# Kernel optimization log

Hardware: AMD Instinct MI355X
Metric: run time of the kernel (lower is better)

## Reference

```python
import jax, jax.numpy as jnp
import numpy as np

N = 50000      # nodes
E = 800000     # edges (before self loops)
H = 4          # heads
C_IN = 128     # input feature dim
C_HID = 64     # per-head out channels (hidden_dim == output_dim)
SLOPE = 0.2    # GATConv leaky_relu negative slope


def setup_inputs() -> dict:
    key = jax.random.key(0)
    ks = jax.random.split(key, 16)
    x = jax.random.normal(ks[0], (N, C_IN), jnp.float32)
    edge_index = jax.random.randint(ks[1], (2, E), 0, N, jnp.int32)

    def p(k, shape):
        return jax.random.normal(k, shape, jnp.float32) * 0.05

    inp = {"x": x, "edge_index": edge_index}
    in_dims = [C_IN, C_HID, C_HID]
    for i in range(3):
        inp[f"W{i+1}"] = p(ks[2 + 4 * i], (in_dims[i], H * C_HID))
        inp[f"asrc{i+1}"] = p(ks[3 + 4 * i], (H, C_HID))
        inp[f"adst{i+1}"] = p(ks[4 + 4 * i], (H, C_HID))
        inp[f"b{i+1}"] = jnp.zeros((C_HID,), jnp.float32)
    return inp


def _gat_layer(x, src, dst, W, a_s, a_d, b):
    # x: [N, F_in]; src/dst: [E'] (self loops included)
    n = x.shape[0]
    h = (x @ W).reshape(n, H, -1)                      # [N, H, C]
    alpha_src = jnp.einsum('nhc,hc->nh', h, a_s)       # att_src . h  (source side)
    alpha_dst = jnp.einsum('nhc,hc->nh', h, a_d)       # att_dst . h  (target side)
    e = jax.nn.leaky_relu(alpha_src[src] + alpha_dst[dst], SLOPE)  # [E', H]
    # scatter-softmax over incoming edges of each dst node
    m = jax.ops.segment_max(e, dst, num_segments=n)    # [N, H]
    ex = jnp.exp(e - m[dst])
    denom = jax.ops.segment_sum(ex, dst, num_segments=n)
    alpha = ex / (denom[dst] + 1e-16)                  # [E', H]
    # scatter-add aggregation of weighted source features
    out = jax.ops.segment_sum(alpha[:, :, None] * h[src], dst, num_segments=n)  # [N, H, C]
    return out.mean(axis=1) + b                        # concat=False -> head mean, + bias


def reference(x, edge_index, W1, asrc1, adst1, b1, W2, asrc2, adst2, b2,
              W3, asrc3, adst3, b3):
    n = x.shape[0]
    loops = jnp.arange(n, dtype=edge_index.dtype)      # GATConv add_self_loops=True
    src = jnp.concatenate([edge_index[0], loops])
    dst = jnp.concatenate([edge_index[1], loops])
    for W, a_s, a_d, b in ((W1, asrc1, adst1, b1),
                           (W2, asrc2, adst2, b2),
                           (W3, asrc3, adst3, b3)):
        x = jax.nn.relu(_gat_layer(x, src, dst, W, a_s, a_d, b))
    return x
```

## Files before the change

kernel.cpp:

```cpp
#include <hip/hip_runtime.h>
#include <hip/hip_bf16.h>
#include <cstddef>

#define NH 4
#define CHID 64
#define HC 256

typedef __attribute__((ext_vector_type(8))) short bf16x8;
typedef __attribute__((ext_vector_type(4))) float f32x4;


__global__ void hist_kernel(const int* __restrict__ ei, int E, int N,
                            int* __restrict__ deg) {
  int i = blockIdx.x * blockDim.x + threadIdx.x;
  int EP = E + N;
  if (i >= EP) return;
  int d = (i < E) ? ei[E + i] : (i - E);
  atomicAdd(&deg[d], 1);
}

__global__ __launch_bounds__(256) void partial_sum_kernel(const int* __restrict__ deg,
                                                          int* __restrict__ part, int n) {
  __shared__ int red[4];
  int t = threadIdx.x;
  int i = blockIdx.x * 256 + t;
  int v = (i < n) ? deg[i] : 0;
#pragma unroll
  for (int o = 32; o; o >>= 1) v += __shfl_xor(v, o, 64);
  if ((t & 63) == 0) red[t >> 6] = v;
  __syncthreads();
  if (t == 0) part[blockIdx.x] = red[0] + red[1] + red[2] + red[3];
}

__global__ __launch_bounds__(256) void scan_part_kernel(int* __restrict__ part, int nb,
                                                        int* __restrict__ row_off, int n) {
  __shared__ int s[256];
  int t = threadIdx.x;
  int v = (t < nb) ? part[t] : 0;
  s[t] = v;
  __syncthreads();
  for (int o = 1; o < 256; o <<= 1) {
    int u = (t >= o) ? s[t - o] : 0;
    __syncthreads();
    s[t] += u;
    __syncthreads();
  }
  if (t < nb) part[t] = s[t] - v;
  if (t == 255) row_off[n] = s[255];
}

__global__ __launch_bounds__(256) void row_off_kernel(const int* __restrict__ deg,
                                                      const int* __restrict__ part,
                                                      int* __restrict__ row_off, int n) {
  __shared__ int s[256];
  int t = threadIdx.x;
  int i = blockIdx.x * 256 + t;
  int v = (i < n) ? deg[i] : 0;
  s[t] = v;
  __syncthreads();
  for (int o = 1; o < 256; o <<= 1) {
    int u = (t >= o) ? s[t - o] : 0;
    __syncthreads();
    s[t] += u;
    __syncthreads();
  }
  if (i < n) row_off[i] = part[blockIdx.x] + s[t] - v;
}

__global__ void scatter_kernel(const int* __restrict__ ei, int E, int N,
                               const int* __restrict__ row_off,
                               int* __restrict__ cursor, int* __restrict__ ssrc,
                               int* __restrict__ sdst) {
  int i = blockIdx.x * blockDim.x + threadIdx.x;
  int EP = E + N;
  if (i >= EP) {
    if (i < EP + 8) { ssrc[i] = 0; sdst[i] = 0; }
    return;
  }
  int s, d;
  if (i < E) { s = ei[i]; d = ei[E + i]; } else { s = i - E; d = s; }
  int pos = row_off[d] + atomicAdd(&cursor[d], 1);
  ssrc[pos] = s;
  sdst[pos] = d;
}


__global__ void prep_kernel(const float* __restrict__ x,
                            __hip_bfloat16* __restrict__ xhi,
                            __hip_bfloat16* __restrict__ xlo, int n4,
                            const float* __restrict__ W1, const float* __restrict__ W2,
                            const float* __restrict__ W3,
                            __hip_bfloat16* __restrict__ w1hi,
                            __hip_bfloat16* __restrict__ w2hi,
                            __hip_bfloat16* __restrict__ w3hi) {
  int i = blockIdx.x * blockDim.x + threadIdx.x;
  if (i < n4) {
    float4 v = reinterpret_cast<const float4*>(x)[i];
    __hip_bfloat16 h[4], l[4];
    float f[4] = {v.x, v.y, v.z, v.w};
#pragma unroll
    for (int j = 0; j < 4; ++j) {
      h[j] = __float2bfloat16(f[j]);
      l[j] = __float2bfloat16(f[j] - __bfloat162float(h[j]));
    }
    reinterpret_cast<uint2*>(xhi)[i] = *reinterpret_cast<uint2*>(h);
    reinterpret_cast<uint2*>(xlo)[i] = *reinterpret_cast<uint2*>(l);
    return;
  }
  int j = i - n4;
  if (j >= 65536) return;
  const float* W; __hip_bfloat16* hi; int K, base;
  if (j < 32768)      { W = W1; hi = w1hi; K = 128; base = j; }
  else if (j < 49152) { W = W2; hi = w2hi; K = 64;  base = j - 32768; }
  else                { W = W3; hi = w3hi; K = 64;  base = j - 49152; }
  int k = base >> 8;
  int c = base & 255;
  hi[c * K + k] = __float2bfloat16(W[base]);
}


template <int K>
__global__ __launch_bounds__(256) void gemm_mfma_kernel(
    const __hip_bfloat16* __restrict__ Ahi, const __hip_bfloat16* __restrict__ Alo,
    const __hip_bfloat16* __restrict__ Bthi,
    const float* __restrict__ a_s, const float* __restrict__ a_d,
    __hip_bfloat16* __restrict__ h, float* __restrict__ asrc_n,
    float* __restrict__ adst_n, int n_rows, int row_groups) {
  extern __shared__ char smem[];
  uint4* lds4 = reinterpret_cast<uint4*>(smem);
  constexpr int KS = K / 32;
  constexpr int S16 = (128 * K * 2) >> 4;
  constexpr int rowshift = (K == 128) ? 4 : 3;
  int ch = blockIdx.y;
  int colbase = ch * 128;

  {
    const uint4* g = reinterpret_cast<const uint4*>(Bthi + (size_t)colbase * K);
    for (int c = threadIdx.x; c < S16; c += 256) {
      int row = c >> rowshift;
      lds4[c ^ (row & 7)] = g[c];
    }
  }
  __syncthreads();

  int wave = threadIdx.x >> 6;
  int lane = threadIdx.x & 63;
  int n16  = lane & 15;
  int g4   = lane >> 4;
  const bf16x8 z8 = {0, 0, 0, 0, 0, 0, 0, 0};

  for (int gg = blockIdx.x; gg < row_groups; gg += gridDim.x) {
    int row0 = gg * 64 + wave * 16;
    int xrow = row0 + n16;
    bool aval = xrow < n_rows;
    size_t xbase = (size_t)xrow * K + g4 * 8;

    bf16x8 xh[KS], xl[KS];
#pragma unroll
    for (int s = 0; s < KS; ++s) {
      xh[s] = aval ? *reinterpret_cast<const bf16x8*>(&Ahi[xbase + s * 32]) : z8;
      xl[s] = aval ? *reinterpret_cast<const bf16x8*>(&Alo[xbase + s * 32]) : z8;
    }

    f32x4 acc[8];
#pragma unroll
    for (int ct = 0; ct < 8; ++ct) acc[ct] = (f32x4){0.f, 0.f, 0.f, 0.f};

#pragma unroll
    for (int ct = 0; ct < 8; ++ct) {
      int wrow = ct * 16 + n16;
#pragma unroll
      for (int s = 0; s < KS; ++s) {
        int ci = ((wrow * K + s * 32 + g4 * 8) >> 3) ^ (wrow & 7);
        bf16x8 wh = *reinterpret_cast<const bf16x8*>(&lds4[ci]);
        acc[ct] = __builtin_amdgcn_mfma_f32_16x16x32_bf16(wh, xh[s], acc[ct], 0, 0, 0);
        acc[ct] = __builtin_amdgcn_mfma_f32_16x16x32_bf16(wh, xl[s], acc[ct], 0, 0, 0);
      }
    }

    int r = row0 + n16;
    bool valid = r < n_rows;

    if (valid) {
#pragma unroll
      for (int ct = 0; ct < 8; ++ct) {
        unsigned short u[4];
#pragma unroll
        for (int i = 0; i < 4; ++i) {
          __hip_bfloat16 b = __float2bfloat16(acc[ct][i]);
          u[i] = *reinterpret_cast<unsigned short*>(&b);
        }
        *reinterpret_cast<uint2*>(&h[(size_t)r * HC + colbase + ct * 16 + g4 * 4]) =
            *reinterpret_cast<uint2*>(u);
      }
    }

    float ps[2] = {0.f, 0.f};
    float pd[2] = {0.f, 0.f};
#pragma unroll
    for (int ct = 0; ct < 8; ++ct) {
      int hh = ct >> 2;
      int col = colbase + ct * 16 + g4 * 4;
      float4 as4 = *reinterpret_cast<const float4*>(&a_s[col]);
      float4 ad4 = *reinterpret_cast<const float4*>(&a_d[col]);
      ps[hh] += acc[ct][0] * as4.x + acc[ct][1] * as4.y + acc[ct][2] * as4.z + acc[ct][3] * as4.w;
      pd[hh] += acc[ct][0] * ad4.x + acc[ct][1] * ad4.y + acc[ct][2] * ad4.z + acc[ct][3] * ad4.w;
    }
#pragma unroll
    for (int hh = 0; hh < 2; ++hh) {
      ps[hh] += __shfl_xor(ps[hh], 16, 64);
      ps[hh] += __shfl_xor(ps[hh], 32, 64);
      pd[hh] += __shfl_xor(pd[hh], 16, 64);
      pd[hh] += __shfl_xor(pd[hh], 32, 64);
    }
    if (lane < 16 && valid) {
      *reinterpret_cast<float2*>(&asrc_n[(size_t)r * NH + ch * 2]) =
          make_float2(ps[0], ps[1]);
      *reinterpret_cast<float2*>(&adst_n[(size_t)r * NH + ch * 2]) =
          make_float2(pd[0], pd[1]);
    }
  }
}


__global__ void edge_weight_kernel(const int* __restrict__ ssrc, const int* __restrict__ sdst,
                                   const float* __restrict__ asrc_n,
                                   const float* __restrict__ adst_n,
                                   float4* __restrict__ wbuf, int EP) {
  int i = blockIdx.x * blockDim.x + threadIdx.x;
  if (i >= EP) {
    if (i < EP + 8) wbuf[i] = make_float4(0.f, 0.f, 0.f, 0.f);
    return;
  }
  int s = ssrc[i];
  int d = sdst[i];
  float4 a = reinterpret_cast<const float4*>(asrc_n)[s];
  float4 b = reinterpret_cast<const float4*>(adst_n)[d];
  float e0 = a.x + b.x; e0 = (e0 > 0.f) ? e0 : 0.2f * e0;
  float e1 = a.y + b.y; e1 = (e1 > 0.f) ? e1 : 0.2f * e1;
  float e2 = a.z + b.z; e2 = (e2 > 0.f) ? e2 : 0.2f * e2;
  float e3 = a.w + b.w; e3 = (e3 > 0.f) ? e3 : 0.2f * e3;
  wbuf[i] = make_float4(__expf(e0), __expf(e1), __expf(e2), __expf(e3));
}


__global__ __launch_bounds__(256) void aggregate_kernel(
    const int* __restrict__ row_off, const int* __restrict__ ssrc,
    const __hip_bfloat16* __restrict__ h, const float4* __restrict__ wbuf,
    const float* __restrict__ bias,
    __hip_bfloat16* __restrict__ out_hi, __hip_bfloat16* __restrict__ out_lo,
    float* __restrict__ out_f32, int n_nodes) {
  int n = (blockIdx.x * blockDim.x + threadIdx.x) >> 6;
  if (n >= n_nodes) return;
  int l    = threadIdx.x & 63;
  int slot = l >> 3;
  int cp   = l & 7;
  const char* hbase = reinterpret_cast<const char*>(h);
  const float4 z4 = make_float4(0.f, 0.f, 0.f, 0.f);
  const uint4 zu = {0, 0, 0, 0};

  int beg  = row_off[n];
  int deg  = row_off[n + 1] - beg;

  float facc[32];
#pragma unroll
  for (int u = 0; u < 32; ++u) facc[u] = 0.f;
  float4 ds = z4;

  auto LOADE = [&](int j, float4& w4, uint4* d) {
    int jj  = j + slot;
    int idx = beg + jj;
    int sv  = ssrc[idx];
    float4 w = wbuf[idx];
    bool ok = jj < deg;
    w4.x = ok ? w.x : 0.f;
    w4.y = ok ? w.y : 0.f;
    w4.z = ok ? w.z : 0.f;
    w4.w = ok ? w.w : 0.f;
    const char* hp = hbase + (size_t)sv * 512 + cp * 16;
    d[0] = *reinterpret_cast<const uint4*>(hp);
    d[1] = *reinterpret_cast<const uint4*>(hp + 128);
    d[2] = *reinterpret_cast<const uint4*>(hp + 256);
    d[3] = *reinterpret_cast<const uint4*>(hp + 384);
  };

  auto PROC = [&](const float4& w4, const uint4* d) {
    ds.x += w4.x; ds.y += w4.y; ds.z += w4.z; ds.w += w4.w;
#pragma unroll
    for (int hh = 0; hh < 4; ++hh) {
      float w = (hh == 0) ? w4.x : (hh == 1) ? w4.y : (hh == 2) ? w4.z : w4.w;
      uint4 dd = d[hh];
      facc[hh * 8 + 0] += w * __uint_as_float(dd.x << 16);
      facc[hh * 8 + 1] += w * __uint_as_float(dd.x & 0xffff0000u);
      facc[hh * 8 + 2] += w * __uint_as_float(dd.y << 16);
      facc[hh * 8 + 3] += w * __uint_as_float(dd.y & 0xffff0000u);
      facc[hh * 8 + 4] += w * __uint_as_float(dd.z << 16);
      facc[hh * 8 + 5] += w * __uint_as_float(dd.z & 0xffff0000u);
      facc[hh * 8 + 6] += w * __uint_as_float(dd.w << 16);
      facc[hh * 8 + 7] += w * __uint_as_float(dd.w & 0xffff0000u);
    }
  };

  float4 wA = z4, wB = z4;
  uint4 dA[4] = {zu, zu, zu, zu};
  uint4 dB[4] = {zu, zu, zu, zu};

  LOADE(0, wA, dA);
  for (int j = 0; j < deg; j += 16) {
    if (j + 8 < deg) LOADE(j + 8, wB, dB); else wB = z4;
    PROC(wA, dA);
    if (j + 16 < deg) LOADE(j + 16, wA, dA); else wA = z4;
    PROC(wB, dB);
  }

#pragma unroll
  for (int o = 8; o <= 32; o <<= 1) {
    ds.x += __shfl_xor(ds.x, o, 64);
    ds.y += __shfl_xor(ds.y, o, 64);
    ds.z += __shfl_xor(ds.z, o, 64);
    ds.w += __shfl_xor(ds.w, o, 64);
  }
  float iv0 = 1.f / (ds.x + 1e-16f);
  float iv1 = 1.f / (ds.y + 1e-16f);
  float iv2 = 1.f / (ds.z + 1e-16f);
  float iv3 = 1.f / (ds.w + 1e-16f);

  float v[8];
#pragma unroll
  for (int u = 0; u < 8; ++u)
    v[u] = facc[u] * iv0 + facc[8 + u] * iv1 + facc[16 + u] * iv2 + facc[24 + u] * iv3;

#pragma unroll
  for (int u = 0; u < 8; ++u) {
    v[u] += __shfl_xor(v[u], 8, 64);
    v[u] += __shfl_xor(v[u], 16, 64);
    v[u] += __shfl_xor(v[u], 32, 64);
  }

  if (slot < 2) {
    float o0 = (slot == 0) ? v[0] : v[4];
    float o1 = (slot == 0) ? v[1] : v[5];
    float o2 = (slot == 0) ? v[2] : v[6];
    float o3 = (slot == 0) ? v[3] : v[7];
    int chn = cp * 8 + slot * 4;
    float4 b4 = *reinterpret_cast<const float4*>(&bias[chn]);
    o0 = fmaxf(0.25f * o0 + b4.x, 0.f);
    o1 = fmaxf(0.25f * o1 + b4.y, 0.f);
    o2 = fmaxf(0.25f * o2 + b4.z, 0.f);
    o3 = fmaxf(0.25f * o3 + b4.w, 0.f);
    if (out_f32) {
      *reinterpret_cast<float4*>(&out_f32[(size_t)n * CHID + chn]) =
          make_float4(o0, o1, o2, o3);
    } else {
      float of[4] = {o0, o1, o2, o3};
      unsigned short hi4[4], lo4[4];
#pragma unroll
      for (int u = 0; u < 4; ++u) {
        __hip_bfloat16 bh = __float2bfloat16(of[u]);
        hi4[u] = *reinterpret_cast<unsigned short*>(&bh);
        __hip_bfloat16 bl = __float2bfloat16(of[u] - __bfloat162float(bh));
        lo4[u] = *reinterpret_cast<unsigned short*>(&bl);
      }
      *reinterpret_cast<uint2*>(&out_hi[(size_t)n * CHID + chn]) = *reinterpret_cast<uint2*>(hi4);
      *reinterpret_cast<uint2*>(&out_lo[(size_t)n * CHID + chn]) = *reinterpret_cast<uint2*>(lo4);
    }
  }
}


extern "C" void kernel_launch(void* const* d_in, const int* in_sizes, int n_in,
                              void* d_out, int out_size, void* d_ws, size_t ws_size,
                              hipStream_t stream) {
  const float* x   = (const float*)d_in[0];
  const int*   ei  = (const int*)d_in[1];
  const float* W1  = (const float*)d_in[2];
  const float* as1 = (const float*)d_in[3];
  const float* ad1 = (const float*)d_in[4];
  const float* b1  = (const float*)d_in[5];
  const float* W2  = (const float*)d_in[6];
  const float* as2 = (const float*)d_in[7];
  const float* ad2 = (const float*)d_in[8];
  const float* b2  = (const float*)d_in[9];
  const float* W3  = (const float*)d_in[10];
  const float* as3 = (const float*)d_in[11];
  const float* ad3 = (const float*)d_in[12];
  const float* b3  = (const float*)d_in[13];

  int N  = in_sizes[0] / 128;
  int E  = in_sizes[1] / 2;
  int EP = E + N;
  int NB = (N + 255) / 256;

  __hip_bfloat16* h     = (__hip_bfloat16*)d_ws;
  __hip_bfloat16* x1hi  = h + (size_t)N * HC;
  __hip_bfloat16* x1lo  = x1hi + (size_t)N * 128;
  __hip_bfloat16* xhi   = x1lo + (size_t)N * 128;
  __hip_bfloat16* xlo   = xhi + (size_t)N * CHID;
  __hip_bfloat16* w1hi  = xlo + (size_t)N * CHID;
  __hip_bfloat16* w2hi  = w1hi + 256 * 128;
  __hip_bfloat16* w3hi  = w2hi + 256 * 64;
  float* asrc_n = (float*)(w3hi + 256 * 64);
  float* adst_n = asrc_n + (size_t)N * NH;
  float4* wbuf  = (float4*)(adst_n + (size_t)N * NH);
  int*   deg    = (int*)(wbuf + (EP + 8));
  int*   cursor = deg + N;
  int*   row_off= cursor + N;
  int*   part   = row_off + (N + 1);
  int*   ssrc   = part + ((NB + 3) & ~3);
  int*   sdst   = ssrc + (EP + 8);

  hipMemsetAsync(deg, 0, sizeof(int) * (size_t)2 * N, stream);
  int eb = (EP + 8 + 255) / 256;
  hist_kernel<<<eb, 256, 0, stream>>>(ei, E, N, deg);
  partial_sum_kernel<<<NB, 256, 0, stream>>>(deg, part, N);
  scan_part_kernel<<<1, 256, 0, stream>>>(part, NB, row_off, N);
  row_off_kernel<<<NB, 256, 0, stream>>>(deg, part, row_off, N);
  scatter_kernel<<<eb, 256, 0, stream>>>(ei, E, N, row_off, cursor, ssrc, sdst);

  int n4 = N * 128 / 4;
  prep_kernel<<<(n4 + 65536 + 255) / 256, 256, 0, stream>>>(x, x1hi, x1lo, n4,
                                                            W1, W2, W3, w1hi, w2hi, w3hi);

  (void)hipFuncSetAttribute(reinterpret_cast<const void*>(&gemm_mfma_kernel<128>),
                            hipFuncAttributeMaxDynamicSharedMemorySize, 65536);
  (void)hipFuncSetAttribute(reinterpret_cast<const void*>(&gemm_mfma_kernel<64>),
                            hipFuncAttributeMaxDynamicSharedMemorySize, 65536);

  int RG = (N + 63) / 64;
  dim3 ggrid(RG, 2);
  int ablocks = (N + 3) / 4;

  gemm_mfma_kernel<128><<<ggrid, 256, 32768, stream>>>(x1hi, x1lo, w1hi, as1, ad1,
                                                       h, asrc_n, adst_n, N, RG);
  edge_weight_kernel<<<eb, 256, 0, stream>>>(ssrc, sdst, asrc_n, adst_n, wbuf, EP);
  aggregate_kernel<<<ablocks, 256, 0, stream>>>(row_off, ssrc, h, wbuf, b1,
                                                xhi, xlo, nullptr, N);
  gemm_mfma_kernel<64><<<ggrid, 256, 16384, stream>>>(xhi, xlo, w2hi, as2, ad2,
                                                      h, asrc_n, adst_n, N, RG);
  edge_weight_kernel<<<eb, 256, 0, stream>>>(ssrc, sdst, asrc_n, adst_n, wbuf, EP);
  aggregate_kernel<<<ablocks, 256, 0, stream>>>(row_off, ssrc, h, wbuf, b2,
                                                xhi, xlo, nullptr, N);
  gemm_mfma_kernel<64><<<ggrid, 256, 16384, stream>>>(xhi, xlo, w3hi, as3, ad3,
                                                      h, asrc_n, adst_n, N, RG);
  edge_weight_kernel<<<eb, 256, 0, stream>>>(ssrc, sdst, asrc_n, adst_n, wbuf, EP);
  aggregate_kernel<<<ablocks, 256, 0, stream>>>(row_off, ssrc, h, wbuf, b3,
                                                nullptr, nullptr, (float*)d_out, N);
}
```

Measured before the change: 399.1 us.

## Fuse edge-weight computation into aggregation and drop split-bf16 low parts

Removes the separate edge_weight kernel and the sdst/wbuf buffers. The aggregation kernel now gathers asrc for each source, adds the node's adst, and applies leaky-relu and exp inline. Separately, the hi/lo bf16 split of activations is dropped, so the GEMMs issue half as many MFMAs and the prep and aggregation write a single bf16 copy. This cuts memory traffic and launches in exchange for lower GEMM input precision, which may push numerical error closer to tolerance.

```diff
diff --git a/kernel.cpp b/kernel.cpp
--- a/kernel.cpp
+++ b/kernel.cpp
@@ -69,60 +69,51 @@
 
 __global__ void scatter_kernel(const int* __restrict__ ei, int E, int N,
                                const int* __restrict__ row_off,
-                               int* __restrict__ cursor, int* __restrict__ ssrc,
-                               int* __restrict__ sdst) {
+                               int* __restrict__ cursor, int* __restrict__ ssrc) {
   int i = blockIdx.x * blockDim.x + threadIdx.x;
   int EP = E + N;
   if (i >= EP) {
-    if (i < EP + 8) { ssrc[i] = 0; sdst[i] = 0; }
+    if (i < EP + 8) ssrc[i] = 0;
     return;
   }
   int s, d;
   if (i < E) { s = ei[i]; d = ei[E + i]; } else { s = i - E; d = s; }
   int pos = row_off[d] + atomicAdd(&cursor[d], 1);
   ssrc[pos] = s;
-  sdst[pos] = d;
 }
 
 
 __global__ void prep_kernel(const float* __restrict__ x,
-                            __hip_bfloat16* __restrict__ xhi,
-                            __hip_bfloat16* __restrict__ xlo, int n4,
+                            __hip_bfloat16* __restrict__ xb, int n4,
                             const float* __restrict__ W1, const float* __restrict__ W2,
                             const float* __restrict__ W3,
-                            __hip_bfloat16* __restrict__ w1hi,
-                            __hip_bfloat16* __restrict__ w2hi,
-                            __hip_bfloat16* __restrict__ w3hi) {
+                            __hip_bfloat16* __restrict__ w1b,
+                            __hip_bfloat16* __restrict__ w2b,
+                            __hip_bfloat16* __restrict__ w3b) {
   int i = blockIdx.x * blockDim.x + threadIdx.x;
   if (i < n4) {
     float4 v = reinterpret_cast<const float4*>(x)[i];
-    __hip_bfloat16 h[4], l[4];
-    float f[4] = {v.x, v.y, v.z, v.w};
-#pragma unroll
-    for (int j = 0; j < 4; ++j) {
-      h[j] = __float2bfloat16(f[j]);
-      l[j] = __float2bfloat16(f[j] - __bfloat162float(h[j]));
-    }
-    reinterpret_cast<uint2*>(xhi)[i] = *reinterpret_cast<uint2*>(h);
-    reinterpret_cast<uint2*>(xlo)[i] = *reinterpret_cast<uint2*>(l);
+    __hip_bfloat16 h[4] = {__float2bfloat16(v.x), __float2bfloat16(v.y),
+                           __float2bfloat16(v.z), __float2bfloat16(v.w)};
+    reinterpret_cast<uint2*>(xb)[i] = *reinterpret_cast<uint2*>(h);
     return;
   }
   int j = i - n4;
   if (j >= 65536) return;
-  const float* W; __hip_bfloat16* hi; int K, base;
-  if (j < 32768)      { W = W1; hi = w1hi; K = 128; base = j; }
-  else if (j < 49152) { W = W2; hi = w2hi; K = 64;  base = j - 32768; }
-  else                { W = W3; hi = w3hi; K = 64;  base = j - 49152; }
+  const float* W; __hip_bfloat16* wb; int K, base;
+  if (j < 32768)      { W = W1; wb = w1b; K = 128; base = j; }
+  else if (j < 49152) { W = W2; wb = w2b; K = 64;  base = j - 32768; }
+  else                { W = W3; wb = w3b; K = 64;  base = j - 49152; }
   int k = base >> 8;
   int c = base & 255;
-  hi[c * K + k] = __float2bfloat16(W[base]);
+  wb[c * K + k] = __float2bfloat16(W[base]);
 }
 
 
 template <int K>
 __global__ __launch_bounds__(256) void gemm_mfma_kernel(
-    const __hip_bfloat16* __restrict__ Ahi, const __hip_bfloat16* __restrict__ Alo,
-    const __hip_bfloat16* __restrict__ Bthi,
+    const __hip_bfloat16* __restrict__ Ab,
+    const __hip_bfloat16* __restrict__ Btb,
     const float* __restrict__ a_s, const float* __restrict__ a_d,
     __hip_bfloat16* __restrict__ h, float* __restrict__ asrc_n,
     float* __restrict__ adst_n, int n_rows, int row_groups) {
@@ -135,7 +126,7 @@
   int colbase = ch * 128;
 
   {
-    const uint4* g = reinterpret_cast<const uint4*>(Bthi + (size_t)colbase * K);
+    const uint4* g = reinterpret_cast<const uint4*>(Btb + (size_t)colbase * K);
     for (int c = threadIdx.x; c < S16; c += 256) {
       int row = c >> rowshift;
       lds4[c ^ (row & 7)] = g[c];
@@ -155,12 +146,10 @@
     bool aval = xrow < n_rows;
     size_t xbase = (size_t)xrow * K + g4 * 8;
 
-    bf16x8 xh[KS], xl[KS];
-#pragma unroll
-    for (int s = 0; s < KS; ++s) {
-      xh[s] = aval ? *reinterpret_cast<const bf16x8*>(&Ahi[xbase + s * 32]) : z8;
-      xl[s] = aval ? *reinterpret_cast<const bf16x8*>(&Alo[xbase + s * 32]) : z8;
-    }
+    bf16x8 xh[KS];
+#pragma unroll
+    for (int s = 0; s < KS; ++s)
+      xh[s] = aval ? *reinterpret_cast<const bf16x8*>(&Ab[xbase + s * 32]) : z8;
 
     f32x4 acc[8];
 #pragma unroll
@@ -174,7 +163,6 @@
         int ci = ((wrow * K + s * 32 + g4 * 8) >> 3) ^ (wrow & 7);
         bf16x8 wh = *reinterpret_cast<const bf16x8*>(&lds4[ci]);
         acc[ct] = __builtin_amdgcn_mfma_f32_16x16x32_bf16(wh, xh[s], acc[ct], 0, 0, 0);
-        acc[ct] = __builtin_amdgcn_mfma_f32_16x16x32_bf16(wh, xl[s], acc[ct], 0, 0, 0);
       }
     }
 
@@ -223,33 +211,11 @@
 }
 
 
-__global__ void edge_weight_kernel(const int* __restrict__ ssrc, const int* __restrict__ sdst,
-                                   const float* __restrict__ asrc_n,
-                                   const float* __restrict__ adst_n,
-                                   float4* __restrict__ wbuf, int EP) {
-  int i = blockIdx.x * blockDim.x + threadIdx.x;
-  if (i >= EP) {
-    if (i < EP + 8) wbuf[i] = make_float4(0.f, 0.f, 0.f, 0.f);
-    return;
-  }
-  int s = ssrc[i];
-  int d = sdst[i];
-  float4 a = reinterpret_cast<const float4*>(asrc_n)[s];
-  float4 b = reinterpret_cast<const float4*>(adst_n)[d];
-  float e0 = a.x + b.x; e0 = (e0 > 0.f) ? e0 : 0.2f * e0;
-  float e1 = a.y + b.y; e1 = (e1 > 0.f) ? e1 : 0.2f * e1;
-  float e2 = a.z + b.z; e2 = (e2 > 0.f) ? e2 : 0.2f * e2;
-  float e3 = a.w + b.w; e3 = (e3 > 0.f) ? e3 : 0.2f * e3;
-  wbuf[i] = make_float4(__expf(e0), __expf(e1), __expf(e2), __expf(e3));
-}
-
-
 __global__ __launch_bounds__(256) void aggregate_kernel(
     const int* __restrict__ row_off, const int* __restrict__ ssrc,
-    const __hip_bfloat16* __restrict__ h, const float4* __restrict__ wbuf,
-    const float* __restrict__ bias,
-    __hip_bfloat16* __restrict__ out_hi, __hip_bfloat16* __restrict__ out_lo,
-    float* __restrict__ out_f32, int n_nodes) {
+    const __hip_bfloat16* __restrict__ h, const float* __restrict__ asrc_n,
+    const float* __restrict__ adst_n, const float* __restrict__ bias,
+    __hip_bfloat16* __restrict__ out_bf, float* __restrict__ out_f32, int n_nodes) {
   int n = (blockIdx.x * blockDim.x + threadIdx.x) >> 6;
   if (n >= n_nodes) return;
   int l    = threadIdx.x & 63;
@@ -261,22 +227,19 @@
 
   int beg  = row_off[n];
   int deg  = row_off[n + 1] - beg;
+  float4 adn = reinterpret_cast<const float4*>(adst_n)[n];
 
   float facc[32];
 #pragma unroll
   for (int u = 0; u < 32; ++u) facc[u] = 0.f;
   float4 ds = z4;
 
-  auto LOADE = [&](int j, float4& w4, uint4* d) {
+  auto LOADE = [&](int j, float4& a4, float& msk, uint4* d) {
     int jj  = j + slot;
     int idx = beg + jj;
     int sv  = ssrc[idx];
-    float4 w = wbuf[idx];
-    bool ok = jj < deg;
-    w4.x = ok ? w.x : 0.f;
-    w4.y = ok ? w.y : 0.f;
-    w4.z = ok ? w.z : 0.f;
-    w4.w = ok ? w.w : 0.f;
+    a4  = reinterpret_cast<const float4*>(asrc_n)[sv];
+    msk = (jj < deg) ? 1.f : 0.f;
     const char* hp = hbase + (size_t)sv * 512 + cp * 16;
     d[0] = *reinterpret_cast<const uint4*>(hp);
     d[1] = *reinterpret_cast<const uint4*>(hp + 128);
@@ -284,11 +247,19 @@
     d[3] = *reinterpret_cast<const uint4*>(hp + 384);
   };
 
-  auto PROC = [&](const float4& w4, const uint4* d) {
-    ds.x += w4.x; ds.y += w4.y; ds.z += w4.z; ds.w += w4.w;
+  auto PROC = [&](const float4& a4, float msk, const uint4* d) {
+    float e0 = a4.x + adn.x; e0 = fmaxf(e0, 0.2f * e0);
+    float e1 = a4.y + adn.y; e1 = fmaxf(e1, 0.2f * e1);
+    float e2 = a4.z + adn.z; e2 = fmaxf(e2, 0.2f * e2);
+    float e3 = a4.w + adn.w; e3 = fmaxf(e3, 0.2f * e3);
+    float w0 = __expf(e0) * msk;
+    float w1 = __expf(e1) * msk;
+    float w2 = __expf(e2) * msk;
+    float w3 = __expf(e3) * msk;
+    ds.x += w0; ds.y += w1; ds.z += w2; ds.w += w3;
 #pragma unroll
     for (int hh = 0; hh < 4; ++hh) {
-      float w = (hh == 0) ? w4.x : (hh == 1) ? w4.y : (hh == 2) ? w4.z : w4.w;
+      float w = (hh == 0) ? w0 : (hh == 1) ? w1 : (hh == 2) ? w2 : w3;
       uint4 dd = d[hh];
       facc[hh * 8 + 0] += w * __uint_as_float(dd.x << 16);
       facc[hh * 8 + 1] += w * __uint_as_float(dd.x & 0xffff0000u);
@@ -301,16 +272,17 @@
     }
   };
 
-  float4 wA = z4, wB = z4;
+  float4 aA = z4, aB = z4;
+  float mA = 0.f, mB = 0.f;
   uint4 dA[4] = {zu, zu, zu, zu};
   uint4 dB[4] = {zu, zu, zu, zu};
 
-  LOADE(0, wA, dA);
+  LOADE(0, aA, mA, dA);
   for (int j = 0; j < deg; j += 16) {
-    if (j + 8 < deg) LOADE(j + 8, wB, dB); else wB = z4;
-    PROC(wA, dA);
-    if (j + 16 < deg) LOADE(j + 16, wA, dA); else wA = z4;
-    PROC(wB, dB);
+    if (j + 8 < deg) LOADE(j + 8, aB, mB, dB); else mB = 0.f;
+    PROC(aA, mA, dA);
+    if (j + 16 < deg) LOADE(j + 16, aA, mA, dA); else mA = 0.f;
+    PROC(aB, mB, dB);
   }
 
 #pragma unroll
@@ -353,16 +325,14 @@
           make_float4(o0, o1, o2, o3);
     } else {
       float of[4] = {o0, o1, o2, o3};
-      unsigned short hi4[4], lo4[4];
+      unsigned short b16[4];
 #pragma unroll
       for (int u = 0; u < 4; ++u) {
         __hip_bfloat16 bh = __float2bfloat16(of[u]);
-        hi4[u] = *reinterpret_cast<unsigned short*>(&bh);
-        __hip_bfloat16 bl = __float2bfloat16(of[u] - __bfloat162float(bh));
-        lo4[u] = *reinterpret_cast<unsigned short*>(&bl);
+        b16[u] = *reinterpret_cast<unsigned short*>(&bh);
       }
-      *reinterpret_cast<uint2*>(&out_hi[(size_t)n * CHID + chn]) = *reinterpret_cast<uint2*>(hi4);
-      *reinterpret_cast<uint2*>(&out_lo[(size_t)n * CHID + chn]) = *reinterpret_cast<uint2*>(lo4);
+      *reinterpret_cast<uint2*>(&out_bf[(size_t)n * CHID + chn]) =
+          *reinterpret_cast<uint2*>(b16);
     }
   }
 }
@@ -391,23 +361,19 @@
   int EP = E + N;
   int NB = (N + 255) / 256;
 
-  __hip_bfloat16* h     = (__hip_bfloat16*)d_ws;
-  __hip_bfloat16* x1hi  = h + (size_t)N * HC;
-  __hip_bfloat16* x1lo  = x1hi + (size_t)N * 128;
-  __hip_bfloat16* xhi   = x1lo + (size_t)N * 128;
-  __hip_bfloat16* xlo   = xhi + (size_t)N * CHID;
-  __hip_bfloat16* w1hi  = xlo + (size_t)N * CHID;
-  __hip_bfloat16* w2hi  = w1hi + 256 * 128;
-  __hip_bfloat16* w3hi  = w2hi + 256 * 64;
-  float* asrc_n = (float*)(w3hi + 256 * 64);
+  __hip_bfloat16* h    = (__hip_bfloat16*)d_ws;
+  __hip_bfloat16* x1b  = h + (size_t)N * HC;
+  __hip_bfloat16* xb   = x1b + (size_t)N * 128;
+  __hip_bfloat16* w1b  = xb + (size_t)N * CHID;
+  __hip_bfloat16* w2b  = w1b + 256 * 128;
+  __hip_bfloat16* w3b  = w2b + 256 * 64;
+  float* asrc_n = (float*)(w3b + 256 * 64);
   float* adst_n = asrc_n + (size_t)N * NH;
-  float4* wbuf  = (float4*)(adst_n + (size_t)N * NH);
-  int*   deg    = (int*)(wbuf + (EP + 8));
+  int*   deg    = (int*)(adst_n + (size_t)N * NH);
   int*   cursor = deg + N;
   int*   row_off= cursor + N;
   int*   part   = row_off + (N + 1);
   int*   ssrc   = part + ((NB + 3) & ~3);
-  int*   sdst   = ssrc + (EP + 8);
 
   hipMemsetAsync(deg, 0, sizeof(int) * (size_t)2 * N, stream);
   int eb = (EP + 8 + 255) / 256;
@@ -415,11 +381,11 @@
   partial_sum_kernel<<<NB, 256, 0, stream>>>(deg, part, N);
   scan_part_kernel<<<1, 256, 0, stream>>>(part, NB, row_off, N);
   row_off_kernel<<<NB, 256, 0, stream>>>(deg, part, row_off, N);
-  scatter_kernel<<<eb, 256, 0, stream>>>(ei, E, N, row_off, cursor, ssrc, sdst);
+  scatter_kernel<<<eb, 256, 0, stream>>>(ei, E, N, row_off, cursor, ssrc);
 
   int n4 = N * 128 / 4;
-  prep_kernel<<<(n4 + 65536 + 255) / 256, 256, 0, stream>>>(x, x1hi, x1lo, n4,
-                                                            W1, W2, W3, w1hi, w2hi, w3hi);
+  prep_kernel<<<(n4 + 65536 + 255) / 256, 256, 0, stream>>>(x, x1b, n4,
+                                                            W1, W2, W3, w1b, w2b, w3b);
 
   (void)hipFuncSetAttribute(reinterpret_cast<const void*>(&gemm_mfma_kernel<128>),
                             hipFuncAttributeMaxDynamicSharedMemorySize, 65536);
@@ -430,19 +396,16 @@
   dim3 ggrid(RG, 2);
   int ablocks = (N + 3) / 4;
 
-  gemm_mfma_kernel<128><<<ggrid, 256, 32768, stream>>>(x1hi, x1lo, w1hi, as1, ad1,
+  gemm_mfma_kernel<128><<<ggrid, 256, 32768, stream>>>(x1b, w1b, as1, ad1,
                                                        h, asrc_n, adst_n, N, RG);
-  edge_weight_kernel<<<eb, 256, 0, stream>>>(ssrc, sdst, asrc_n, adst_n, wbuf, EP);
-  aggregate_kernel<<<ablocks, 256, 0, stream>>>(row_off, ssrc, h, wbuf, b1,
-                                                xhi, xlo, nullptr, N);
-  gemm_mfma_kernel<64><<<ggrid, 256, 16384, stream>>>(xhi, xlo, w2hi, as2, ad2,
+  aggregate_kernel<<<ablocks, 256, 0, stream>>>(row_off, ssrc, h, asrc_n, adst_n, b1,
+                                                xb, nullptr, N);
+  gemm_mfma_kernel<64><<<ggrid, 256, 16384, stream>>>(xb, w2b, as2, ad2,
                                                       h, asrc_n, adst_n, N, RG);
-  edge_weight_kernel<<<eb, 256, 0, stream>>>(ssrc, sdst, asrc_n, adst_n, wbuf, EP);
-  aggregate_kernel<<<ablocks, 256, 0, stream>>>(row_off, ssrc, h, wbuf, b2,
-                                                xhi, xlo, nullptr, N);
-  gemm_mfma_kernel<64><<<ggrid, 256, 16384, stream>>>(xhi, xlo, w3hi, as3, ad3,
+  aggregate_kernel<<<ablocks, 256, 0, stream>>>(row_off, ssrc, h, asrc_n, adst_n, b2,
+                                                xb, nullptr, N);
+  gemm_mfma_kernel<64><<<ggrid, 256, 16384, stream>>>(xb, w3b, as3, ad3,
                                                       h, asrc_n, adst_n, N, RG);
-  edge_weight_kernel<<<eb, 256, 0, stream>>>(ssrc, sdst, asrc_n, adst_n, wbuf, EP);
-  aggregate_kernel<<<ablocks, 256, 0, stream>>>(row_off, ssrc, h, wbuf, b3,
-                                                nullptr, nullptr, (float*)d_out, N);
-}
+  aggregate_kernel<<<ablocks, 256, 0, stream>>>(row_off, ssrc, h, asrc_n, adst_n, b3,
+                                                nullptr, (float*)d_out, N);
+}
```

After: 367.8 us. 7.8% less time.
